# Kernel tuning notes

Hardware: AMD Instinct MI355X
Metric: run time of the kernel (lower is better)

The kernel has to match this reference:

```python
import jax, jax.numpy as jnp
import numpy as np

N_NODES = 100000
N_EDGES = 1000000
IN_CH = 64
HID = 64
PROJ = 128
N_GRAPHS = 64
BN_EPS = 1e-5


def _glorot(key, shape):
    fan_in, fan_out = shape[0], shape[1]
    lim = (6.0 / (fan_in + fan_out)) ** 0.5
    return jax.random.uniform(key, shape, jnp.float32, -lim, lim)


def setup_inputs() -> dict:
    key = jax.random.key(0)
    ks = jax.random.split(key, 16)
    x = jax.random.normal(ks[0], (N_NODES, IN_CH), jnp.float32)
    edge_index = jax.random.randint(ks[1], (2, N_EDGES), 0, N_NODES, jnp.int64)
    batch = jnp.sort(jax.random.randint(ks[2], (N_NODES,), 0, N_GRAPHS, jnp.int64))
    inp = {
        "x": x, "edge_index": edge_index, "batch": batch,
        # conv1 MLP: Linear(2*in, hid), Linear(hid, hid)
        "c1_w1": _glorot(ks[3], (2 * IN_CH, HID)), "c1_b1": jnp.zeros((HID,), jnp.float32),
        "c1_w2": _glorot(ks[4], (HID, HID)), "c1_b2": jnp.zeros((HID,), jnp.float32),
        "bn1_g": jnp.ones((HID,), jnp.float32), "bn1_b": jnp.zeros((HID,), jnp.float32),
        # conv2 MLP: Linear(2*hid, hid), Linear(hid, hid)
        "c2_w1": _glorot(ks[5], (2 * HID, HID)), "c2_b1": jnp.zeros((HID,), jnp.float32),
        "c2_w2": _glorot(ks[6], (HID, HID)), "c2_b2": jnp.zeros((HID,), jnp.float32),
        "bn2_g": jnp.ones((HID,), jnp.float32), "bn2_b": jnp.zeros((HID,), jnp.float32),
        # projector: Linear(2*hid, proj), BN(proj), Linear(proj, proj)
        "p_w1": _glorot(ks[7], (2 * HID, PROJ)), "p_b1": jnp.zeros((PROJ,), jnp.float32),
        "p_bng": jnp.ones((PROJ,), jnp.float32), "p_bnb": jnp.zeros((PROJ,), jnp.float32),
        "p_w2": _glorot(ks[8], (PROJ, PROJ)), "p_b2": jnp.zeros((PROJ,), jnp.float32),
    }
    return inp


def _edge_conv(x, src, dst, w1, b1, w2, b2):
    # PyG EdgeConv: message = nn(cat([x_i, x_j - x_i])), aggr = max over incoming edges
    xi = x[dst]                                   # [E, C] target features
    xj = x[src]                                   # [E, C] source features
    m = jnp.concatenate([xi, xj - xi], axis=-1)   # [E, 2C]
    h = jax.nn.relu(m @ w1 + b1)
    h = jax.nn.relu(h @ w2 + b2)                  # [E, H]
    out = jax.ops.segment_max(h, dst, num_segments=N_NODES)
    return jnp.where(jnp.isfinite(out), out, 0.0)  # nodes w/o in-edges -> 0


def _batchnorm(x, g, b):
    mu = jnp.mean(x, axis=0)
    var = jnp.mean((x - mu) ** 2, axis=0)  # biased var (training-mode BN)
    return (x - mu) * jax.lax.rsqrt(var + BN_EPS) * g + b


def reference(x, edge_index, batch,
              c1_w1, c1_b1, c1_w2, c1_b2, bn1_g, bn1_b,
              c2_w1, c2_b1, c2_w2, c2_b2, bn2_g, bn2_b,
              p_w1, p_b1, p_bng, p_bnb, p_w2, p_b2):
    src, dst = edge_index[0], edge_index[1]
    h = _edge_conv(x, src, dst, c1_w1, c1_b1, c1_w2, c1_b2)
    h = _batchnorm(h, bn1_g, bn1_b)
    h = _edge_conv(h, src, dst, c2_w1, c2_b1, c2_w2, c2_b2)
    x_node = _batchnorm(h, bn2_g, bn2_b)            # [N, H]
    # graph pooling
    counts = jax.ops.segment_sum(jnp.ones((N_NODES,), x_node.dtype), batch,
                                 num_segments=N_GRAPHS)
    mean_pool = jax.ops.segment_sum(x_node, batch, num_segments=N_GRAPHS) / \
        jnp.maximum(counts, 1.0)[:, None]
    max_pool = jax.ops.segment_max(x_node, batch, num_segments=N_GRAPHS)
    max_pool = jnp.where(jnp.isfinite(max_pool), max_pool, 0.0)
    x_graph = jnp.concatenate([mean_pool, max_pool], axis=1)  # [G, 2H]
    # projector MLP
    z = x_graph @ p_w1 + p_b1
    z = jax.nn.relu(_batchnorm(z, p_bng, p_bnb))
    z_proj = z @ p_w2 + p_b2                        # [G, PROJ]
    return (z_proj, x_node, x_graph)
```

## Files before the change

kernel.cpp:

```cpp
#include <hip/hip_runtime.h>
#include <hip/hip_fp16.h>

constexpr int NN = 100000;
constexpr int NE = 1000000;
constexpr int NG = 64;
constexpr float BN_EPS = 1e-5f;
constexpr int NTILES = NE / 32;
constexpr int NNTILES = NN / 32;
constexpr int NREC = NTILES * 2;

constexpr int NBUK = 196;
constexpr int BINB = 256;
constexpr int BCHUNK = (NE + BINB - 1) / BINB;
constexpr int TABN = NBUK * BINB;

constexpr long H1R_OFF  = 0;
constexpr long XNR_OFF  = 3200000;
constexpr long PART_OFF = 6400000;
constexpr long SC1_OFF  = PART_OFF + 32768;
constexpr long SH1_OFF  = SC1_OFF + 64;
constexpr long SC2_OFF  = SH1_OFF + 64;
constexpr long SH2_OFF  = SC2_OFF + 64;
constexpr long PSUM_OFF = SH2_OFF + 64;
constexpr long PMAX_OFF = PSUM_OFF + 4096;
constexpr long CNT_OFF  = PMAX_OFF + 4096;
constexpr long TICK_OFF = CNT_OFF + 64;
constexpr long TAB_OFF  = TICK_OFF + 16;
constexpr long SEDG_OFF = TAB_OFF + 50176;
constexpr long WF1_OFF  = SEDG_OFF + 2000000;
constexpr long WF2_OFF  = WF1_OFF + 6144;
constexpr long RECD_OFF = WF2_OFF + 6144;
constexpr long RECV_OFF = RECD_OFF + 62528;
constexpr long P_OFF    = RECV_OFF + 2000000;
constexpr long Q_OFF    = P_OFF + 3200000;

constexpr long OUT_XNODE = 8192;
constexpr long OUT_XG    = 8192 + 6400000L;

using f16x8 = __attribute__((ext_vector_type(8))) _Float16;
using f32x16 = __attribute__((ext_vector_type(16))) float;

__device__ __forceinline__ unsigned short f2h(float f) {
    return __builtin_bit_cast(unsigned short, (_Float16)f);
}
__device__ __forceinline__ unsigned pkrtz(float a, float b) {
    return __builtin_bit_cast(unsigned, __builtin_amdgcn_cvt_pkrtz(a, b));
}
__device__ __forceinline__ unsigned pk_add_f16(unsigned a, unsigned b) {
    unsigned d;
    asm("v_pk_add_f16 %0, %1, %2" : "=v"(d) : "v"(a), "v"(b));
    return d;
}
__device__ __forceinline__ unsigned pk_max_f16(unsigned a, unsigned b) {
    unsigned d;
    asm("v_pk_max_f16 %0, %1, %2" : "=v"(d) : "v"(a), "v"(b));
    return d;
}
__device__ __forceinline__ float h2f_lo(unsigned u) {
    return (float)__builtin_bit_cast(_Float16, (unsigned short)(u & 0xffffu));
}
__device__ __forceinline__ float h2f_hi(unsigned u) {
    return (float)__builtin_bit_cast(_Float16, (unsigned short)(u >> 16));
}
__device__ __forceinline__ unsigned fenc(float f) {
    unsigned u = __float_as_uint(f);
    return (u & 0x80000000u) ? ~u : (u | 0x80000000u);
}
__device__ __forceinline__ float fdec(unsigned u) {
    return (u & 0x80000000u) ? __uint_as_float(u & 0x7fffffffu) : __uint_as_float(~u);
}
__device__ __forceinline__ int xcd_swz(int bid, int nwg) {
    const int q = nwg >> 3, r = nwg & 7;
    const int x = bid & 7, i = bid >> 3;
    return (x < r ? x * (q + 1) : r * (q + 1) + (x - r) * q) + i;
}

__global__ __launch_bounds__(256) void bin_hist_kernel(
    const int* __restrict__ dst, int* __restrict__ tab, int* __restrict__ ticket)
{
    __shared__ int cnt[NBUK];
    __shared__ int part[256];
    __shared__ int flag;
    const int t = threadIdx.x, b = blockIdx.x;
    if (t < NBUK) cnt[t] = 0;
    __syncthreads();
    const int lo = b * BCHUNK;
    const int hi = (lo + BCHUNK < NE) ? lo + BCHUNK : NE;
    for (int e = lo + t; e < hi; e += 256) atomicAdd(&cnt[dst[e] >> 9], 1);
    __syncthreads();
    if (t < NBUK) tab[t * BINB + b] = cnt[t];
    __syncthreads();
    if (t == 0) {
        __threadfence();
        flag = (atomicAdd(ticket, 1) == BINB - 1) ? 1 : 0;
    }
    __syncthreads();
    if (!flag) return;
    __threadfence();
    constexpr int STRIP = TABN / 256;
    int s = 0;
    for (int i = 0; i < STRIP; ++i) s += tab[t * STRIP + i];
    part[t] = s;
    __syncthreads();
    for (int off = 1; off < 256; off <<= 1) {
        const int u = (t >= off) ? part[t - off] : 0;
        __syncthreads();
        part[t] += u;
        __syncthreads();
    }
    int run = (t == 0) ? 0 : part[t - 1];
    for (int i = 0; i < STRIP; ++i) {
        const int v = tab[t * STRIP + i];
        tab[t * STRIP + i] = run;
        run += v;
    }
}

__global__ __launch_bounds__(256) void bin_scatter_kernel(
    const int* __restrict__ src, const int* __restrict__ dst,
    const int* __restrict__ tab, int2* __restrict__ ebin)
{
    __shared__ int basec[NBUK];
    __shared__ int cur[NBUK];
    const int t = threadIdx.x, b = blockIdx.x;
    if (t < NBUK) { basec[t] = tab[t * BINB + b]; cur[t] = 0; }
    __syncthreads();
    const int lo = b * BCHUNK;
    const int hi = (lo + BCHUNK < NE) ? lo + BCHUNK : NE;
    for (int e = lo + t; e < hi; e += 256) {
        const int d = dst[e];
        const int k = d >> 9;
        const int pos = basec[k] + atomicAdd(&cur[k], 1);
        ebin[pos] = make_int2(src[e], d);
    }
}

__global__ __launch_bounds__(256) void bucket_sort_kernel(
    const int2* __restrict__ ebin, const int* __restrict__ tab,
    int2* __restrict__ sedge)
{
    __shared__ int hist[512];
    __shared__ int part[256];
    const int t = threadIdx.x, k = blockIdx.x;
    const int start = tab[k * BINB];
    const int end = (k == NBUK - 1) ? NE : tab[(k + 1) * BINB];
    hist[t * 2] = 0; hist[t * 2 + 1] = 0;
    __syncthreads();
    for (int e = start + t; e < end; e += 256) atomicAdd(&hist[ebin[e].y & 511], 1);
    __syncthreads();
    const int v0 = hist[t * 2], v1 = hist[t * 2 + 1];
    part[t] = v0 + v1;
    __syncthreads();
    for (int off = 1; off < 256; off <<= 1) {
        const int u = (t >= off) ? part[t - off] : 0;
        __syncthreads();
        part[t] += u;
        __syncthreads();
    }
    int run = (t == 0) ? 0 : part[t - 1];
    hist[t * 2] = run;
    hist[t * 2 + 1] = run + v0;
    __syncthreads();
    for (int e = start + t; e < end; e += 256) {
        const int2 v = ebin[e];
        const int pos = start + atomicAdd(&hist[v.y & 511], 1);
        sedge[pos] = v;
    }
}

__global__ __launch_bounds__(256) void prep_weights(
    const float* __restrict__ c1w1, const float* __restrict__ c1w2,
    const float* __restrict__ c2w1, const float* __restrict__ c2w2,
    unsigned short* __restrict__ wf)
{
    const int gidx = blockIdx.x * 256 + threadIdx.x;
    if (gidx >= 24576) return;
    const bool second = gidx >= 12288;
    const int idx = second ? gidx - 12288 : gidx;
    const float* __restrict__ w1 = second ? c2w1 : c1w1;
    const float* __restrict__ w2 = second ? c2w2 : c1w2;
    const int sec = idx >> 12;
    const int j = idx & 4095;
    const int f = j >> 9, rem = j & 511, ln = rem >> 3, i = rem & 7;
    const int t = f >> 2, ks = f & 3;
    const int k = ks * 16 + (ln >> 5) * 8 + i, c = t * 32 + (ln & 31);
    float v;
    if (sec == 0)      v = w1[k * 64 + c] - w1[(64 + k) * 64 + c];
    else if (sec == 1) v = w1[(64 + k) * 64 + c];
    else               v = w2[k * 64 + c];
    wf[gidx] = f2h(v);
}

template<bool NORM>
__global__ __launch_bounds__(256) void nodegemm_kernel(
    const void* __restrict__ xin,
    const unsigned short* __restrict__ wfrag,
    const float* __restrict__ b1,
    const float* __restrict__ scale, const float* __restrict__ shift,
    unsigned short* __restrict__ P, unsigned short* __restrict__ Q)
{
    __shared__ unsigned short wlds[8192];
    {
        const uint4* wsrc = reinterpret_cast<const uint4*>(wfrag);
        uint4* wdst = reinterpret_cast<uint4*>(wlds);
        #pragma unroll
        for (int i = 0; i < 4; ++i) wdst[threadIdx.x + i * 256] = wsrc[threadIdx.x + i * 256];
    }
    __syncthreads();

    const int wid = threadIdx.x >> 6, lane = threadIdx.x & 63;
    const int hi = lane >> 5, ln32 = lane & 31;
    const int tile = blockIdx.x * 4 + wid;
    if (tile >= NNTILES) return;
    const int node = tile * 32 + ln32;

    f32x16 cpa, cpb, cqa, cqb;
    #pragma unroll
    for (int r = 0; r < 16; ++r) {
        const int row = (r & 3) + 8 * (r >> 2) + 4 * hi;
        cpa[r] = b1[row]; cpb[r] = b1[32 + row];
        cqa[r] = 0.f;     cqb[r] = 0.f;
    }

    #pragma unroll
    for (int ks = 0; ks < 4; ++ks) {
        const int off = ks * 16 + hi * 8;
        float4 a, b;
        if constexpr (!NORM) {
            const float* xr = reinterpret_cast<const float*>(xin) + (long)node * 64;
            a = *reinterpret_cast<const float4*>(xr + off);
            b = *reinterpret_cast<const float4*>(xr + off + 4);
        } else {
            const unsigned* xr = reinterpret_cast<const unsigned*>(xin) + (long)node * 32;
            const uint4 u = *reinterpret_cast<const uint4*>(xr + ks * 8 + hi * 4);
            a.x = h2f_lo(u.x); a.y = h2f_hi(u.x); a.z = h2f_lo(u.y); a.w = h2f_hi(u.y);
            b.x = h2f_lo(u.z); b.y = h2f_hi(u.z); b.z = h2f_lo(u.w); b.w = h2f_hi(u.w);
            const float4 s0 = *reinterpret_cast<const float4*>(scale + off);
            const float4 s1 = *reinterpret_cast<const float4*>(scale + off + 4);
            const float4 h0 = *reinterpret_cast<const float4*>(shift + off);
            const float4 h1 = *reinterpret_cast<const float4*>(shift + off + 4);
            a.x = fmaf(a.x, s0.x, h0.x); a.y = fmaf(a.y, s0.y, h0.y);
            a.z = fmaf(a.z, s0.z, h0.z); a.w = fmaf(a.w, s0.w, h0.w);
            b.x = fmaf(b.x, s1.x, h1.x); b.y = fmaf(b.y, s1.y, h1.y);
            b.z = fmaf(b.z, s1.z, h1.z); b.w = fmaf(b.w, s1.w, h1.w);
        }
        uint4 uu;
        uu.x = pkrtz(a.x, a.y); uu.y = pkrtz(a.z, a.w);
        uu.z = pkrtz(b.x, b.y); uu.w = pkrtz(b.z, b.w);
        const f16x8 bfr = __builtin_bit_cast(f16x8, uu);
        const f16x8 ap0 = *reinterpret_cast<const f16x8*>(&wlds[(0 * 4 + ks) * 512 + lane * 8]);
        const f16x8 ap1 = *reinterpret_cast<const f16x8*>(&wlds[(1 * 4 + ks) * 512 + lane * 8]);
        const f16x8 aq0 = *reinterpret_cast<const f16x8*>(&wlds[4096 + (0 * 4 + ks) * 512 + lane * 8]);
        const f16x8 aq1 = *reinterpret_cast<const f16x8*>(&wlds[4096 + (1 * 4 + ks) * 512 + lane * 8]);
        cpa = __builtin_amdgcn_mfma_f32_32x32x16_f16(ap0, bfr, cpa, 0, 0, 0);
        cpb = __builtin_amdgcn_mfma_f32_32x32x16_f16(ap1, bfr, cpb, 0, 0, 0);
        cqa = __builtin_amdgcn_mfma_f32_32x32x16_f16(aq0, bfr, cqa, 0, 0, 0);
        cqb = __builtin_amdgcn_mfma_f32_32x32x16_f16(aq1, bfr, cqb, 0, 0, 0);
    }

    unsigned short* Pr = P + (long)node * 64;
    unsigned short* Qr = Q + (long)node * 64;
    #pragma unroll
    for (int t = 0; t < 2; ++t) {
        const f32x16 cp = t ? cpb : cpa;
        const f32x16 cq = t ? cqb : cqa;
        #pragma unroll
        for (int g2 = 0; g2 < 4; ++g2) {
            uint2 up, uq;
            up.x = pkrtz(cp[4 * g2 + 0], cp[4 * g2 + 1]);
            up.y = pkrtz(cp[4 * g2 + 2], cp[4 * g2 + 3]);
            uq.x = pkrtz(cq[4 * g2 + 0], cq[4 * g2 + 1]);
            uq.y = pkrtz(cq[4 * g2 + 2], cq[4 * g2 + 3]);
            const int co = t * 32 + 8 * g2 + 4 * hi;
            *reinterpret_cast<uint2*>(Pr + co) = up;
            *reinterpret_cast<uint2*>(Qr + co) = uq;
        }
    }
}

__global__ __launch_bounds__(256) void edgeconv_kernel(
    const unsigned short* __restrict__ P, const unsigned short* __restrict__ Q,
    const int2* __restrict__ sedge,
    const unsigned short* __restrict__ w2frag,
    const float* __restrict__ b2,
    unsigned* __restrict__ out,
    int* __restrict__ recd, unsigned* __restrict__ recv)
{
    __shared__ unsigned short wlds[4096];
    {
        const uint4* wsrc = reinterpret_cast<const uint4*>(w2frag);
        uint4* wdst = reinterpret_cast<uint4*>(wlds);
        #pragma unroll
        for (int i = 0; i < 2; ++i) wdst[threadIdx.x + i * 256] = wsrc[threadIdx.x + i * 256];
    }
    __syncthreads();

    const int wid  = threadIdx.x >> 6;
    const int lane = threadIdx.x & 63;
    const int hi   = lane >> 5;
    const int ln32 = lane & 31;
    const int tile = xcd_swz(blockIdx.x, gridDim.x) * 4 + wid;
    if (tile >= NTILES) return;

    const int2 sd = sedge[tile * 32 + ln32];
    const int s = sd.x, d = sd.y;
    const unsigned short* __restrict__ Pr = P + (long)d * 64;
    const unsigned short* __restrict__ Qr = Q + (long)s * 64;

    uint4 pu[4], qu[4];
    #pragma unroll
    for (int ks = 0; ks < 4; ++ks) {
        const int co = ks * 16 + hi * 8;
        pu[ks] = *reinterpret_cast<const uint4*>(Pr + co);
        qu[ks] = *reinterpret_cast<const uint4*>(Qr + co);
    }

    f32x16 c2a, c2b;
    #pragma unroll
    for (int r = 0; r < 16; ++r) {
        const int row = (r & 3) + 8 * (r >> 2) + 4 * hi;
        c2a[r] = b2[row];
        c2b[r] = b2[32 + row];
    }

    #pragma unroll
    for (int ks = 0; ks < 4; ++ks) {
        uint4 hh;
        hh.x = pk_max_f16(pk_add_f16(pu[ks].x, qu[ks].x), 0u);
        hh.y = pk_max_f16(pk_add_f16(pu[ks].y, qu[ks].y), 0u);
        hh.z = pk_max_f16(pk_add_f16(pu[ks].z, qu[ks].z), 0u);
        hh.w = pk_max_f16(pk_add_f16(pu[ks].w, qu[ks].w), 0u);
        const f16x8 bfr = __builtin_bit_cast(f16x8, hh);
        const f16x8 a0 = *reinterpret_cast<const f16x8*>(&wlds[(0 * 4 + ks) * 512 + lane * 8]);
        const f16x8 a1 = *reinterpret_cast<const f16x8*>(&wlds[(1 * 4 + ks) * 512 + lane * 8]);
        c2a = __builtin_amdgcn_mfma_f32_32x32x16_f16(a0, bfr, c2a, 0, 0, 0);
        c2b = __builtin_amdgcn_mfma_f32_32x32x16_f16(a1, bfr, c2b, 0, 0, 0);
    }

    unsigned pkc[16];
    #pragma unroll
    for (int q = 0; q < 8; ++q) {
        pkc[q]     = pk_max_f16(pkrtz(c2a[2 * q], c2a[2 * q + 1]), 0u);
        pkc[8 + q] = pk_max_f16(pkrtz(c2b[2 * q], c2b[2 * q + 1]), 0u);
    }

    #pragma unroll
    for (int st = 1; st < 32; st <<= 1) {
        const int dn = __shfl_down(d, st, 32);
        const bool take = (ln32 + st < 32) && (dn == d);
        #pragma unroll
        for (int i = 0; i < 16; ++i) {
            const unsigned o = __shfl_down(pkc[i], st, 32);
            const unsigned m = pk_max_f16(pkc[i], o);
            pkc[i] = take ? m : pkc[i];
        }
    }
    const int dprev = __shfl_up(d, 1, 32);
    const bool leader = (ln32 == 0) || (d != dprev);
    const unsigned lm = (unsigned)(__ballot(leader) & 0xffffffffull);
    const int L31 = 31 - __builtin_clz(lm);

    if (leader) {
        if (ln32 != 0 && ln32 != L31) {
            unsigned* row = out + (long)d * 32;
            #pragma unroll
            for (int g2 = 0; g2 < 4; ++g2) {
                *reinterpret_cast<uint2*>(row + 4 * g2 + 2 * hi) =
                    make_uint2(pkc[2 * g2], pkc[2 * g2 + 1]);
                *reinterpret_cast<uint2*>(row + 16 + 4 * g2 + 2 * hi) =
                    make_uint2(pkc[8 + 2 * g2], pkc[8 + 2 * g2 + 1]);
            }
        }
        if (ln32 == 0) {
            unsigned* row = recv + (long)(tile * 2) * 32;
            #pragma unroll
            for (int g2 = 0; g2 < 4; ++g2) {
                *reinterpret_cast<uint2*>(row + 4 * g2 + 2 * hi) =
                    make_uint2(pkc[2 * g2], pkc[2 * g2 + 1]);
                *reinterpret_cast<uint2*>(row + 16 + 4 * g2 + 2 * hi) =
                    make_uint2(pkc[8 + 2 * g2], pkc[8 + 2 * g2 + 1]);
            }
            if (hi == 0) recd[tile * 2] = d;
        }
        if (ln32 == L31) {
            unsigned* row = recv + (long)(tile * 2 + 1) * 32;
            #pragma unroll
            for (int g2 = 0; g2 < 4; ++g2) {
                *reinterpret_cast<uint2*>(row + 4 * g2 + 2 * hi) =
                    make_uint2(pkc[2 * g2], pkc[2 * g2 + 1]);
                *reinterpret_cast<uint2*>(row + 16 + 4 * g2 + 2 * hi) =
                    make_uint2(pkc[8 + 2 * g2], pkc[8 + 2 * g2 + 1]);
            }
            if (hi == 0) recd[tile * 2 + 1] = d;
        }
    }
}

__global__ __launch_bounds__(256) void fixup_kernel(
    const int* __restrict__ recd, const unsigned* __restrict__ recv,
    unsigned* __restrict__ out)
{
    const int wid = threadIdx.x >> 6;
    const int half = (threadIdx.x >> 5) & 1;
    const int c2 = threadIdx.x & 31;
    const int r = blockIdx.x * 8 + wid * 2 + half;
    if (r >= NREC) return;
    const int d = recd[r];
    int lo = r, hi = r;
    while (lo > 0 && recd[lo - 1] == d) --lo;
    while (hi + 1 < NREC && recd[hi + 1] == d) ++hi;
    unsigned m = 0u;
    for (int rr = lo; rr <= hi; ++rr) m = pk_max_f16(m, recv[(long)rr * 32 + c2]);
    out[(long)d * 32 + c2] = m;
}

__global__ __launch_bounds__(256) void stats_kernel(
    const unsigned* __restrict__ h, float* __restrict__ partial,
    const float* __restrict__ g, const float* __restrict__ b,
    float* __restrict__ scale, float* __restrict__ shift, int* __restrict__ ticket)
{
    __shared__ float red[4][256];
    __shared__ float red2[2][256];
    __shared__ int flag;
    const int tid = threadIdx.x;
    const int c2 = tid & 31, r = tid >> 5;
    float s0 = 0.f, ss0 = 0.f, s1 = 0.f, ss1 = 0.f;
    for (int v = blockIdx.x * 8 + r; v < NN; v += 256 * 8) {
        const unsigned u = h[(long)v * 32 + c2];
        const float a = h2f_lo(u), bb = h2f_hi(u);
        s0 += a; ss0 += a * a; s1 += bb; ss1 += bb * bb;
    }
    red[0][tid] = s0; red[1][tid] = ss0; red[2][tid] = s1; red[3][tid] = ss1;
    __syncthreads();
    if (r == 0) {
        float S0 = 0.f, SS0 = 0.f, S1 = 0.f, SS1 = 0.f;
        #pragma unroll
        for (int q = 0; q < 8; ++q) {
            S0 += red[0][c2 + q * 32]; SS0 += red[1][c2 + q * 32];
            S1 += red[2][c2 + q * 32]; SS1 += red[3][c2 + q * 32];
        }
        partial[blockIdx.x * 128 + 2 * c2]     = S0;
        partial[blockIdx.x * 128 + 2 * c2 + 1] = S1;
        partial[blockIdx.x * 128 + 64 + 2 * c2]     = SS0;
        partial[blockIdx.x * 128 + 64 + 2 * c2 + 1] = SS1;
    }
    __syncthreads();
    if (tid == 0) {
        __threadfence();
        flag = (atomicAdd(ticket, 1) == 255) ? 1 : 0;
    }
    __syncthreads();
    if (!flag) return;
    __threadfence();
    const int c = tid & 63, q = tid >> 6;
    float S = 0.f, SS = 0.f;
    for (int bb2 = q * 64; bb2 < q * 64 + 64; ++bb2) {
        S += partial[bb2 * 128 + c];
        SS += partial[bb2 * 128 + 64 + c];
    }
    red2[0][tid] = S; red2[1][tid] = SS;
    __syncthreads();
    if (q == 0) {
        #pragma unroll
        for (int p = 1; p < 4; ++p) { S += red2[0][c + p * 64]; SS += red2[1][c + p * 64]; }
        const float invN = 1.0f / (float)NN;
        const float mu = S * invN;
        const float var = SS * invN - mu * mu;
        const float sc = g[c] * rsqrtf(var + BN_EPS);
        scale[c] = sc;
        shift[c] = b[c] - mu * sc;
    }
}

constexpr int NPB = 256;
__global__ __launch_bounds__(256) void nodepass_kernel(
    const unsigned* __restrict__ xnr, float* __restrict__ xn,
    const int* __restrict__ batch,
    const float* __restrict__ scale, const float* __restrict__ shift,
    float* __restrict__ poolsum, unsigned* __restrict__ poolmax, int* __restrict__ counts)
{
    const int base = blockIdx.x * NPB;
    const int r = threadIdx.x >> 5, c2 = threadIdx.x & 31;
    const float sc0 = scale[2 * c2], sc1 = scale[2 * c2 + 1];
    const float sh0 = shift[2 * c2], sh1 = shift[2 * c2 + 1];
    int curg = -1; float rs0 = 0.f, rs1 = 0.f, rm0 = -INFINITY, rm1 = -INFINITY; int rc = 0;
    const int vend = (base + NPB < NN) ? base + NPB : NN;
    for (int v = base + r; v < vend; v += 8) {
        const unsigned u = xnr[(long)v * 32 + c2];
        const float v0 = fmaf(h2f_lo(u), sc0, sh0);
        const float v1 = fmaf(h2f_hi(u), sc1, sh1);
        *reinterpret_cast<float2*>(xn + (long)v * 64 + 2 * c2) = make_float2(v0, v1);
        const int g = batch[v];
        if (g != curg) {
            if (curg >= 0) {
                atomicAdd(poolsum + curg * 64 + 2 * c2, rs0);
                atomicAdd(poolsum + curg * 64 + 2 * c2 + 1, rs1);
                atomicMax(poolmax + curg * 64 + 2 * c2, fenc(rm0));
                atomicMax(poolmax + curg * 64 + 2 * c2 + 1, fenc(rm1));
                if (c2 == 0) atomicAdd(counts + curg, rc);
            }
            curg = g; rs0 = rs1 = 0.f; rm0 = rm1 = -INFINITY; rc = 0;
        }
        rs0 += v0; rs1 += v1; rm0 = fmaxf(rm0, v0); rm1 = fmaxf(rm1, v1); ++rc;
    }
    if (curg >= 0) {
        atomicAdd(poolsum + curg * 64 + 2 * c2, rs0);
        atomicAdd(poolsum + curg * 64 + 2 * c2 + 1, rs1);
        atomicMax(poolmax + curg * 64 + 2 * c2, fenc(rm0));
        atomicMax(poolmax + curg * 64 + 2 * c2 + 1, fenc(rm1));
        if (c2 == 0) atomicAdd(counts + curg, rc);
    }
}

__global__ __launch_bounds__(1024) void final_kernel(
    const float* __restrict__ poolsum, const unsigned* __restrict__ poolmax,
    const int* __restrict__ counts,
    const float* __restrict__ p_w1, const float* __restrict__ p_b1,
    const float* __restrict__ p_bng, const float* __restrict__ p_bnb,
    const float* __restrict__ p_w2, const float* __restrict__ p_b2,
    float* __restrict__ out)
{
    __shared__ float xg[64][128];
    __shared__ float znl[64 * 129];
    __shared__ float red[2][1024];
    __shared__ float scsh[2][128];
    const int tid = threadIdx.x;

    #pragma unroll
    for (int i = 0; i < 8; ++i) {
        const int e2 = tid + i * 1024;
        const int g = e2 >> 7, col = e2 & 127;
        float val;
        if (col < 64) {
            const float cnt = fmaxf((float)counts[g], 1.f);
            val = poolsum[g * 64 + col] / cnt;
        } else {
            const unsigned u = poolmax[g * 64 + col - 64];
            val = (u == 0u) ? 0.f : fdec(u);
        }
        xg[g][col] = val;
        out[OUT_XG + e2] = val;
    }
    __syncthreads();

    const int gg = tid >> 7, t = tid & 127;
    float z[8];
    #pragma unroll
    for (int gi = 0; gi < 8; ++gi) z[gi] = p_b1[t];
    for (int j = 0; j < 128; ++j) {
        const float wv = p_w1[j * 128 + t];
        #pragma unroll
        for (int gi = 0; gi < 8; ++gi) z[gi] = fmaf(xg[gg * 8 + gi][j], wv, z[gi]);
    }

    float s = 0.f, ss = 0.f;
    #pragma unroll
    for (int gi = 0; gi < 8; ++gi) { s += z[gi]; ss += z[gi] * z[gi]; }
    red[0][tid] = s; red[1][tid] = ss;
    __syncthreads();
    if (gg == 0) {
        float S = 0.f, SS = 0.f;
        #pragma unroll
        for (int q = 0; q < 8; ++q) { S += red[0][t + q * 128]; SS += red[1][t + q * 128]; }
        const float mu = S / 64.f;
        const float var = SS / 64.f - mu * mu;
        const float sc = p_bng[t] * rsqrtf(var + BN_EPS);
        scsh[0][t] = sc;
        scsh[1][t] = p_bnb[t] - mu * sc;
    }
    __syncthreads();
    const float sc = scsh[0][t], sh = scsh[1][t];
    #pragma unroll
    for (int gi = 0; gi < 8; ++gi) {
        const float zn = fmaxf(fmaf(z[gi], sc, sh), 0.f);
        znl[(gg * 8 + gi) * 129 + t] = zn;
    }
    __syncthreads();

    float zp[8];
    #pragma unroll
    for (int gi = 0; gi < 8; ++gi) zp[gi] = p_b2[t];
    for (int c = 0; c < 128; ++c) {
        const float wv = p_w2[c * 128 + t];
        #pragma unroll
        for (int gi = 0; gi < 8; ++gi) zp[gi] = fmaf(znl[(gg * 8 + gi) * 129 + c], wv, zp[gi]);
    }
    #pragma unroll
    for (int gi = 0; gi < 8; ++gi) out[(gg * 8 + gi) * 128 + t] = zp[gi];
}

extern "C" void kernel_launch(void* const* d_in, const int* in_sizes, int n_in,
                              void* d_out, int out_size, void* d_ws, size_t ws_size,
                              hipStream_t stream)
{
    const float* x     = (const float*)d_in[0];
    const int*   eidx  = (const int*)d_in[1];
    const int*   batch = (const int*)d_in[2];
    const float* c1w1  = (const float*)d_in[3];
    const float* c1b1  = (const float*)d_in[4];
    const float* c1w2  = (const float*)d_in[5];
    const float* c1b2  = (const float*)d_in[6];
    const float* bn1g  = (const float*)d_in[7];
    const float* bn1b  = (const float*)d_in[8];
    const float* c2w1  = (const float*)d_in[9];
    const float* c2b1  = (const float*)d_in[10];
    const float* c2w2  = (const float*)d_in[11];
    const float* c2b2  = (const float*)d_in[12];
    const float* bn2g  = (const float*)d_in[13];
    const float* bn2b  = (const float*)d_in[14];
    const float* pw1   = (const float*)d_in[15];
    const float* pb1   = (const float*)d_in[16];
    const float* pbng  = (const float*)d_in[17];
    const float* pbnb  = (const float*)d_in[18];
    const float* pw2   = (const float*)d_in[19];
    const float* pb2   = (const float*)d_in[20];

    const int* src = eidx;
    const int* dst = eidx + NE;

    float* ws  = (float*)d_ws;
    float* o   = (float*)d_out;
    unsigned* h1r = (unsigned*)(ws + H1R_OFF);
    unsigned* xnr = (unsigned*)(ws + XNR_OFF);
    float* xnode = o + OUT_XNODE;
    int* tick  = (int*)(ws + TICK_OFF);
    int* tab   = (int*)(ws + TAB_OFF);
    int2* ebin  = (int2*)(ws + H1R_OFF);
    int2* sedge = (int2*)(ws + SEDG_OFF);
    unsigned short* wf1 = (unsigned short*)(ws + WF1_OFF);
    unsigned short* wf2 = (unsigned short*)(ws + WF2_OFF);
    int* recd  = (int*)(ws + RECD_OFF);
    unsigned* recv = (unsigned*)(ws + RECV_OFF);
    unsigned short* Pb = (unsigned short*)(ws + P_OFF);
    unsigned short* Qb = (unsigned short*)(ws + Q_OFF);

    hipMemsetAsync(ws + PSUM_OFF, 0, (4096 + 4096 + 64 + 16) * 4, stream);

    prep_weights<<<96, 256, 0, stream>>>(c1w1, c1w2, c2w1, c2w2, wf1);

    bin_hist_kernel<<<BINB, 256, 0, stream>>>(dst, tab, tick + 0);
    bin_scatter_kernel<<<BINB, 256, 0, stream>>>(src, dst, tab, ebin);
    bucket_sort_kernel<<<NBUK, 256, 0, stream>>>(ebin, tab, sedge);

    hipMemsetAsync(h1r, 0, (size_t)NN * 64 * 2 * 2, stream);

    const int ngGrid   = (NNTILES + 3) / 4;
    const int convGrid = (NTILES + 3) / 4;
    const int fixGrid  = (NREC + 7) / 8;

    nodegemm_kernel<false><<<ngGrid, 256, 0, stream>>>(
        x, wf1, c1b1, nullptr, nullptr, Pb, Qb);
    edgeconv_kernel<<<convGrid, 256, 0, stream>>>(
        Pb, Qb, sedge, wf1 + 8192, c1b2, h1r, recd, recv);
    fixup_kernel<<<fixGrid, 256, 0, stream>>>(recd, recv, h1r);
    stats_kernel<<<256, 256, 0, stream>>>(h1r, ws + PART_OFF, bn1g, bn1b,
                                          ws + SC1_OFF, ws + SH1_OFF, tick + 1);
    nodegemm_kernel<true><<<ngGrid, 256, 0, stream>>>(
        h1r, wf2, c2b1, ws + SC1_OFF, ws + SH1_OFF, Pb, Qb);
    edgeconv_kernel<<<convGrid, 256, 0, stream>>>(
        Pb, Qb, sedge, wf2 + 8192, c2b2, xnr, recd, recv);
    fixup_kernel<<<fixGrid, 256, 0, stream>>>(recd, recv, xnr);
    stats_kernel<<<256, 256, 0, stream>>>(xnr, ws + PART_OFF, bn2g, bn2b,
                                          ws + SC2_OFF, ws + SH2_OFF, tick + 2);
    nodepass_kernel<<<(NN + NPB - 1) / NPB, 256, 0, stream>>>(
        xnr, xnode, batch, ws + SC2_OFF, ws + SH2_OFF,
        ws + PSUM_OFF, (unsigned*)(ws + PMAX_OFF), (int*)(ws + CNT_OFF));
    final_kernel<<<1, 1024, 0, stream>>>(
        ws + PSUM_OFF, (unsigned*)(ws + PMAX_OFF), (int*)(ws + CNT_OFF),
        pw1, pb1, pbng, pbnb, pw2, pb2, o);
}
```

Measured before the change: 373.6 us.

## Process several edge tiles per wave and move table scan into a separate kernel

The edge-conv kernel now loops over four 32-edge tiles per wave, so the grid shrinks and the weight fragments staged into LDS once per block are reused across more edges. The P/Q loads are also moved inside the MFMA loop instead of being fully prefetched up front. Separately, the last-block ticket scan in the histogram kernel is replaced by a single 1024-thread scan kernel that keeps values in registers. Fewer tiles in flight per wave and the serial tile loop may reduce latency hiding on the gather loads, and the scan adds one more kernel launch.

```diff
diff --git a/kernel.cpp b/kernel.cpp
--- a/kernel.cpp
+++ b/kernel.cpp
@@ -8,6 +8,7 @@
 constexpr int NTILES = NE / 32;
 constexpr int NNTILES = NN / 32;
 constexpr int NREC = NTILES * 2;
+constexpr int TPW = 4;
 
 constexpr int NBUK = 196;
 constexpr int BINB = 256;
@@ -76,11 +77,9 @@
 }
 
 __global__ __launch_bounds__(256) void bin_hist_kernel(
-    const int* __restrict__ dst, int* __restrict__ tab, int* __restrict__ ticket)
+    const int* __restrict__ dst, int* __restrict__ tab)
 {
     __shared__ int cnt[NBUK];
-    __shared__ int part[256];
-    __shared__ int flag;
     const int t = threadIdx.x, b = blockIdx.x;
     if (t < NBUK) cnt[t] = 0;
     __syncthreads();
@@ -89,30 +88,35 @@
     for (int e = lo + t; e < hi; e += 256) atomicAdd(&cnt[dst[e] >> 9], 1);
     __syncthreads();
     if (t < NBUK) tab[t * BINB + b] = cnt[t];
-    __syncthreads();
-    if (t == 0) {
-        __threadfence();
-        flag = (atomicAdd(ticket, 1) == BINB - 1) ? 1 : 0;
-    }
-    __syncthreads();
-    if (!flag) return;
-    __threadfence();
-    constexpr int STRIP = TABN / 256;
+}
+
+__global__ __launch_bounds__(1024) void scan_tab_kernel(int* __restrict__ tab)
+{
+    __shared__ int part[1024];
+    const int t = threadIdx.x;
+    constexpr int VPT = 49;
+    int vals[VPT];
+    const int base = t * VPT;
     int s = 0;
-    for (int i = 0; i < STRIP; ++i) s += tab[t * STRIP + i];
+    #pragma unroll
+    for (int i = 0; i < VPT; ++i) {
+        const int idx = base + i;
+        const int v = (idx < TABN) ? tab[idx] : 0;
+        vals[i] = v; s += v;
+    }
     part[t] = s;
     __syncthreads();
-    for (int off = 1; off < 256; off <<= 1) {
+    for (int off = 1; off < 1024; off <<= 1) {
         const int u = (t >= off) ? part[t - off] : 0;
         __syncthreads();
         part[t] += u;
         __syncthreads();
     }
     int run = (t == 0) ? 0 : part[t - 1];
-    for (int i = 0; i < STRIP; ++i) {
-        const int v = tab[t * STRIP + i];
-        tab[t * STRIP + i] = run;
-        run += v;
+    #pragma unroll
+    for (int i = 0; i < VPT; ++i) {
+        const int idx = base + i;
+        if (idx < TABN) { const int v = vals[i]; tab[idx] = run; run += v; }
     }
 }
 
@@ -299,99 +303,99 @@
     const int lane = threadIdx.x & 63;
     const int hi   = lane >> 5;
     const int ln32 = lane & 31;
-    const int tile = xcd_swz(blockIdx.x, gridDim.x) * 4 + wid;
-    if (tile >= NTILES) return;
-
-    const int2 sd = sedge[tile * 32 + ln32];
-    const int s = sd.x, d = sd.y;
-    const unsigned short* __restrict__ Pr = P + (long)d * 64;
-    const unsigned short* __restrict__ Qr = Q + (long)s * 64;
-
-    uint4 pu[4], qu[4];
-    #pragma unroll
-    for (int ks = 0; ks < 4; ++ks) {
-        const int co = ks * 16 + hi * 8;
-        pu[ks] = *reinterpret_cast<const uint4*>(Pr + co);
-        qu[ks] = *reinterpret_cast<const uint4*>(Qr + co);
-    }
-
-    f32x16 c2a, c2b;
-    #pragma unroll
-    for (int r = 0; r < 16; ++r) {
-        const int row = (r & 3) + 8 * (r >> 2) + 4 * hi;
-        c2a[r] = b2[row];
-        c2b[r] = b2[32 + row];
-    }
-
-    #pragma unroll
-    for (int ks = 0; ks < 4; ++ks) {
-        uint4 hh;
-        hh.x = pk_max_f16(pk_add_f16(pu[ks].x, qu[ks].x), 0u);
-        hh.y = pk_max_f16(pk_add_f16(pu[ks].y, qu[ks].y), 0u);
-        hh.z = pk_max_f16(pk_add_f16(pu[ks].z, qu[ks].z), 0u);
-        hh.w = pk_max_f16(pk_add_f16(pu[ks].w, qu[ks].w), 0u);
-        const f16x8 bfr = __builtin_bit_cast(f16x8, hh);
-        const f16x8 a0 = *reinterpret_cast<const f16x8*>(&wlds[(0 * 4 + ks) * 512 + lane * 8]);
-        const f16x8 a1 = *reinterpret_cast<const f16x8*>(&wlds[(1 * 4 + ks) * 512 + lane * 8]);
-        c2a = __builtin_amdgcn_mfma_f32_32x32x16_f16(a0, bfr, c2a, 0, 0, 0);
-        c2b = __builtin_amdgcn_mfma_f32_32x32x16_f16(a1, bfr, c2b, 0, 0, 0);
-    }
-
-    unsigned pkc[16];
-    #pragma unroll
-    for (int q = 0; q < 8; ++q) {
-        pkc[q]     = pk_max_f16(pkrtz(c2a[2 * q], c2a[2 * q + 1]), 0u);
-        pkc[8 + q] = pk_max_f16(pkrtz(c2b[2 * q], c2b[2 * q + 1]), 0u);
-    }
-
-    #pragma unroll
-    for (int st = 1; st < 32; st <<= 1) {
-        const int dn = __shfl_down(d, st, 32);
-        const bool take = (ln32 + st < 32) && (dn == d);
-        #pragma unroll
-        for (int i = 0; i < 16; ++i) {
-            const unsigned o = __shfl_down(pkc[i], st, 32);
-            const unsigned m = pk_max_f16(pkc[i], o);
-            pkc[i] = take ? m : pkc[i];
-        }
-    }
-    const int dprev = __shfl_up(d, 1, 32);
-    const bool leader = (ln32 == 0) || (d != dprev);
-    const unsigned lm = (unsigned)(__ballot(leader) & 0xffffffffull);
-    const int L31 = 31 - __builtin_clz(lm);
-
-    if (leader) {
-        if (ln32 != 0 && ln32 != L31) {
-            unsigned* row = out + (long)d * 32;
+    const int tile0 = (xcd_swz(blockIdx.x, gridDim.x) * 4 + wid) * TPW;
+
+    #pragma unroll 1
+    for (int tt = 0; tt < TPW; ++tt) {
+        const int tile = tile0 + tt;
+        if (tile >= NTILES) break;
+
+        const int2 sd = sedge[tile * 32 + ln32];
+        const int s = sd.x, d = sd.y;
+        const unsigned short* __restrict__ Pr = P + (long)d * 64;
+        const unsigned short* __restrict__ Qr = Q + (long)s * 64;
+
+        f32x16 c2a, c2b;
+        #pragma unroll
+        for (int r = 0; r < 16; ++r) {
+            const int row = (r & 3) + 8 * (r >> 2) + 4 * hi;
+            c2a[r] = b2[row];
+            c2b[r] = b2[32 + row];
+        }
+
+        #pragma unroll
+        for (int ks = 0; ks < 4; ++ks) {
+            const int co = ks * 16 + hi * 8;
+            const uint4 pu = *reinterpret_cast<const uint4*>(Pr + co);
+            const uint4 qu = *reinterpret_cast<const uint4*>(Qr + co);
+            uint4 hh;
+            hh.x = pk_max_f16(pk_add_f16(pu.x, qu.x), 0u);
+            hh.y = pk_max_f16(pk_add_f16(pu.y, qu.y), 0u);
+            hh.z = pk_max_f16(pk_add_f16(pu.z, qu.z), 0u);
+            hh.w = pk_max_f16(pk_add_f16(pu.w, qu.w), 0u);
+            const f16x8 bfr = __builtin_bit_cast(f16x8, hh);
+            const f16x8 a0 = *reinterpret_cast<const f16x8*>(&wlds[(0 * 4 + ks) * 512 + lane * 8]);
+            const f16x8 a1 = *reinterpret_cast<const f16x8*>(&wlds[(1 * 4 + ks) * 512 + lane * 8]);
+            c2a = __builtin_amdgcn_mfma_f32_32x32x16_f16(a0, bfr, c2a, 0, 0, 0);
+            c2b = __builtin_amdgcn_mfma_f32_32x32x16_f16(a1, bfr, c2b, 0, 0, 0);
+        }
+
+        unsigned pkc[16];
+        #pragma unroll
+        for (int q = 0; q < 8; ++q) {
+            pkc[q]     = pk_max_f16(pkrtz(c2a[2 * q], c2a[2 * q + 1]), 0u);
+            pkc[8 + q] = pk_max_f16(pkrtz(c2b[2 * q], c2b[2 * q + 1]), 0u);
+        }
+
+        #pragma unroll
+        for (int st = 1; st < 32; st <<= 1) {
+            const int dn = __shfl_down(d, st, 32);
+            const bool take = (ln32 + st < 32) && (dn == d);
             #pragma unroll
-            for (int g2 = 0; g2 < 4; ++g2) {
-                *reinterpret_cast<uint2*>(row + 4 * g2 + 2 * hi) =
-                    make_uint2(pkc[2 * g2], pkc[2 * g2 + 1]);
-                *reinterpret_cast<uint2*>(row + 16 + 4 * g2 + 2 * hi) =
-                    make_uint2(pkc[8 + 2 * g2], pkc[8 + 2 * g2 + 1]);
+            for (int i = 0; i < 16; ++i) {
+                const unsigned o = __shfl_down(pkc[i], st, 32);
+                const unsigned m = pk_max_f16(pkc[i], o);
+                pkc[i] = take ? m : pkc[i];
             }
         }
-        if (ln32 == 0) {
-            unsigned* row = recv + (long)(tile * 2) * 32;
-            #pragma unroll
-            for (int g2 = 0; g2 < 4; ++g2) {
-                *reinterpret_cast<uint2*>(row + 4 * g2 + 2 * hi) =
-                    make_uint2(pkc[2 * g2], pkc[2 * g2 + 1]);
-                *reinterpret_cast<uint2*>(row + 16 + 4 * g2 + 2 * hi) =
-                    make_uint2(pkc[8 + 2 * g2], pkc[8 + 2 * g2 + 1]);
+        const int dprev = __shfl_up(d, 1, 32);
+        const bool leader = (ln32 == 0) || (d != dprev);
+        const unsigned lm = (unsigned)(__ballot(leader) & 0xffffffffull);
+        const int L31 = 31 - __builtin_clz(lm);
+
+        if (leader) {
+            if (ln32 != 0 && ln32 != L31) {
+                unsigned* row = out + (long)d * 32;
+                #pragma unroll
+                for (int g2 = 0; g2 < 4; ++g2) {
+                    *reinterpret_cast<uint2*>(row + 4 * g2 + 2 * hi) =
+                        make_uint2(pkc[2 * g2], pkc[2 * g2 + 1]);
+                    *reinterpret_cast<uint2*>(row + 16 + 4 * g2 + 2 * hi) =
+                        make_uint2(pkc[8 + 2 * g2], pkc[8 + 2 * g2 + 1]);
+                }
             }
-            if (hi == 0) recd[tile * 2] = d;
-        }
-        if (ln32 == L31) {
-            unsigned* row = recv + (long)(tile * 2 + 1) * 32;
-            #pragma unroll
-            for (int g2 = 0; g2 < 4; ++g2) {
-                *reinterpret_cast<uint2*>(row + 4 * g2 + 2 * hi) =
-                    make_uint2(pkc[2 * g2], pkc[2 * g2 + 1]);
-                *reinterpret_cast<uint2*>(row + 16 + 4 * g2 + 2 * hi) =
-                    make_uint2(pkc[8 + 2 * g2], pkc[8 + 2 * g2 + 1]);
+            if (ln32 == 0) {
+                unsigned* row = recv + (long)(tile * 2) * 32;
+                #pragma unroll
+                for (int g2 = 0; g2 < 4; ++g2) {
+                    *reinterpret_cast<uint2*>(row + 4 * g2 + 2 * hi) =
+                        make_uint2(pkc[2 * g2], pkc[2 * g2 + 1]);
+                    *reinterpret_cast<uint2*>(row + 16 + 4 * g2 + 2 * hi) =
+                        make_uint2(pkc[8 + 2 * g2], pkc[8 + 2 * g2 + 1]);
+                }
+                if (hi == 0) recd[tile * 2] = d;
             }
-            if (hi == 0) recd[tile * 2 + 1] = d;
+            if (ln32 == L31) {
+                unsigned* row = recv + (long)(tile * 2 + 1) * 32;
+                #pragma unroll
+                for (int g2 = 0; g2 < 4; ++g2) {
+                    *reinterpret_cast<uint2*>(row + 4 * g2 + 2 * hi) =
+                        make_uint2(pkc[2 * g2], pkc[2 * g2 + 1]);
+                    *reinterpret_cast<uint2*>(row + 16 + 4 * g2 + 2 * hi) =
+                        make_uint2(pkc[8 + 2 * g2], pkc[8 + 2 * g2 + 1]);
+                }
+                if (hi == 0) recd[tile * 2 + 1] = d;
+            }
         }
     }
 }
@@ -638,14 +642,15 @@
 
     prep_weights<<<96, 256, 0, stream>>>(c1w1, c1w2, c2w1, c2w2, wf1);
 
-    bin_hist_kernel<<<BINB, 256, 0, stream>>>(dst, tab, tick + 0);
+    bin_hist_kernel<<<BINB, 256, 0, stream>>>(dst, tab);
+    scan_tab_kernel<<<1, 1024, 0, stream>>>(tab);
     bin_scatter_kernel<<<BINB, 256, 0, stream>>>(src, dst, tab, ebin);
     bucket_sort_kernel<<<NBUK, 256, 0, stream>>>(ebin, tab, sedge);
 
     hipMemsetAsync(h1r, 0, (size_t)NN * 64 * 2 * 2, stream);
 
     const int ngGrid   = (NNTILES + 3) / 4;
-    const int convGrid = (NTILES + 3) / 4;
+    const int convGrid = (NTILES + 4 * TPW - 1) / (4 * TPW);
     const int fixGrid  = (NREC + 7) / 8;
 
     nodegemm_kernel<false><<<ngGrid, 256, 0, stream>>>(
```

Measured after the change: 368.4 us. Within noise of the previous version (-1.4%).
